# Kernel optimization log

Hardware: AMD Instinct MI355X
Metric: run time of the kernel (lower is better)

Reference implementation:

```python
import jax, jax.numpy as jnp
import numpy as np

NUM_SEQS = 4
SEQ_LEN = 2048
T = NUM_SEQS * SEQ_LEN          # total tokens
D_IN = 4096
D_OUT = 4096
NUM_ADAPTERS = 8
MAX_RANK = 64
CACHE_LEN = NUM_ADAPTERS * MAX_RANK  # 512 pages


def setup_inputs() -> dict:
    key = jax.random.key(0)
    ks = jax.random.split(key, 8)
    x = jax.random.normal(ks[0], (T, D_IN), dtype=jnp.float32)
    weight = jax.random.normal(ks[1], (D_OUT, D_IN), dtype=jnp.float32) * 0.02
    bias = jax.random.normal(ks[2], (D_OUT,), dtype=jnp.float32) * 0.02
    a_cache = jax.random.normal(ks[3], (CACHE_LEN, D_IN), dtype=jnp.float32) * 0.02
    b_cache = jax.random.normal(ks[4], (CACHE_LEN, D_OUT), dtype=jnp.float32) * 0.02
    b_start_loc = (jnp.arange(NUM_SEQS) * SEQ_LEN).astype(jnp.int32)
    b_adapter_ids = jax.random.randint(ks[5], (NUM_SEQS,), 0, NUM_ADAPTERS).astype(jnp.int32)
    b_scaling = jax.random.uniform(ks[6], (NUM_SEQS,), dtype=jnp.float32, minval=0.5, maxval=2.0)
    # page i for (adapter a, rank slot r) lives at a*MAX_RANK + r
    rank_page_table = jnp.arange(CACHE_LEN, dtype=jnp.int32).reshape(NUM_ADAPTERS, MAX_RANK)
    ranks = jax.random.randint(ks[7], (NUM_ADAPTERS,), 1, MAX_RANK + 1).astype(jnp.int32)
    return {"x": x, "weight": weight, "bias": bias, "a_cache": a_cache,
            "b_cache": b_cache, "b_start_loc": b_start_loc,
            "b_adapter_ids": b_adapter_ids, "b_scaling": b_scaling,
            "rank_page_table": rank_page_table, "ranks": ranks}


def reference(x, weight, bias, a_cache, b_cache, b_start_loc,
              b_adapter_ids, b_scaling, rank_page_table, ranks):
    t = x.shape[0]
    num_adapters, max_rank = rank_page_table.shape
    # map each token to its sequence -> adapter id / scaling (mbgmm dispatch)
    seg = jnp.searchsorted(b_start_loc, jnp.arange(t, dtype=b_start_loc.dtype),
                           side='right') - 1                      # [T]
    tok_adapter = b_adapter_ids[seg]                              # [T]
    tok_scale = b_scaling[seg]                                    # [T]
    # gather paged LoRA A/B weights per adapter: [A, R, D]
    A_all = a_cache[rank_page_table]                              # [A, R, D_in]
    B_all = b_cache[rank_page_table]                              # [A, R, D_out]
    # mbgmm_a: xa[t, r] = x[t] . A[adapter(t), r], zero beyond rank
    xa_all = jnp.einsum('td,ard->tar', x, A_all)                  # [T, A, R]
    rmask = (jnp.arange(max_rank)[None, :] < ranks[:, None])      # [A, R]
    onehot = (tok_adapter[:, None] == jnp.arange(num_adapters)[None, :])  # [T, A]
    sel = (onehot[:, :, None] & rmask[None, :, :]).astype(x.dtype)  # [T, A, R]
    xa_sel = xa_all * sel
    # mbgmm_b: lora_out[t] = scaling * sum_r xa[t, r] * B[adapter(t), r]
    lora_out = jnp.einsum('tar,aro->to', xa_sel, B_all) * tok_scale[:, None]
    base_out = x @ weight.T + bias
    return base_out + lora_out
```

## Files before the change

kernel.cpp:

```cpp
#include <hip/hip_runtime.h>
#include <hip/hip_bf16.h>

typedef unsigned short u16;
typedef unsigned int u32;
typedef __attribute__((ext_vector_type(8))) short bf16x8;
typedef __attribute__((ext_vector_type(4))) float f32x4;

#define T_TOK 8192
#define DIN 4096
#define DOUT 4096
#define N_SEQS 4
#define N_ADPT 8
#define MAXR 64
#define CACHE_LEN 512

__device__ __forceinline__ u16 f2bf(float f) {
    u32 u = __builtin_bit_cast(u32, f);
    u += 0x7fffu + ((u >> 16) & 1u);
    return (u16)(u >> 16);
}

__device__ __forceinline__ void load_lds16(const u16* g, u16* l) {
    __builtin_amdgcn_global_load_lds(
        (const __attribute__((address_space(1))) u32*)g,
        (__attribute__((address_space(3))) u32*)l, 16, 0, 0);
}

__global__ void cvt_kernel(const float* __restrict__ in, u16* __restrict__ out, int n4) {
    int i = blockIdx.x * blockDim.x + threadIdx.x;
    int stride = gridDim.x * blockDim.x;
    for (; i < n4; i += stride) {
        float4 v = reinterpret_cast<const float4*>(in)[i];
        ushort4 o;
        o.x = f2bf(v.x); o.y = f2bf(v.y); o.z = f2bf(v.z); o.w = f2bf(v.w);
        reinterpret_cast<ushort4*>(out)[i] = o;
    }
}

__global__ void build_bt(const float* __restrict__ b_cache, const int* __restrict__ rpt,
                         u16* __restrict__ Bt) {
    int id = blockIdx.x * 256 + threadIdx.x;
    int n  = id & (DOUT - 1);
    int rb = (id >> 12) & 7;
    int a  = id >> 15;
    union { u16 u[8]; uint4 v; } pack;
    #pragma unroll
    for (int j = 0; j < 8; ++j) {
        int r = rb * 8 + j;
        int page = rpt[a * MAXR + r];
        pack.u[j] = f2bf(b_cache[(long)page * DOUT + n]);
    }
    *reinterpret_cast<uint4*>(&Bt[((long)(a * DOUT + n)) * MAXR + rb * 8]) = pack.v;
}

__launch_bounds__(256)
__global__ void xa_kernel(const u16* __restrict__ xb, const u16* __restrict__ ab,
                          const int* __restrict__ b_start_loc,
                          const int* __restrict__ b_adapter_ids,
                          const float* __restrict__ b_scaling,
                          const int* __restrict__ rpt,
                          const int* __restrict__ ranks,
                          u16* __restrict__ xa) {
    int t0 = blockIdx.x * 128;
    int seg = 0;
    #pragma unroll
    for (int i = 1; i < N_SEQS; ++i) if (b_start_loc[i] <= t0) seg = i;
    int adapter = b_adapter_ids[seg];
    float scale = b_scaling[seg];
    int rank = ranks[adapter];

    __shared__ __attribute__((aligned(16))) u16 As[128 * 32];
    __shared__ __attribute__((aligned(16))) u16 Bs[64 * 32];

    int tid = threadIdx.x;
    int lane = tid & 63, wave = tid >> 6;
    int lr = lane & 15, lk = lane >> 4;

    int e0 = wave * 64 + lane;
    int e1 = 256 + e0;
    int ra0 = e0 >> 2, ca0 = (e0 & 3) * 8;
    int ra1 = e1 >> 2, ca1 = (e1 & 3) * 8;
    const u16* gA0 = xb + (long)(t0 + ra0) * DIN + ca0;
    const u16* gA1 = xb + (long)(t0 + ra1) * DIN + ca1;
    int rB = ra0;
    int page = rpt[adapter * MAXR + rB];
    const u16* gB = ab + (long)page * DIN + ca0;

    f32x4 acc[2][4] = {};

    for (int k0 = 0; k0 < DIN; k0 += 32) {
        load_lds16(gA0 + k0, As + wave * 512);
        load_lds16(gA1 + k0, As + 2048 + wave * 512);
        load_lds16(gB + k0,  Bs + wave * 512);
        asm volatile("s_waitcnt vmcnt(0)" ::: "memory");
        __syncthreads();
        bf16x8 af[2], bfr[4];
        #pragma unroll
        for (int m = 0; m < 2; ++m)
            af[m] = *(const bf16x8*)&As[(wave * 32 + m * 16 + lr) * 32 + lk * 8];
        #pragma unroll
        for (int n = 0; n < 4; ++n)
            bfr[n] = *(const bf16x8*)&Bs[(n * 16 + lr) * 32 + lk * 8];
        #pragma unroll
        for (int m = 0; m < 2; ++m)
            #pragma unroll
            for (int n = 0; n < 4; ++n)
                acc[m][n] = __builtin_amdgcn_mfma_f32_16x16x32_bf16(af[m], bfr[n], acc[m][n], 0, 0, 0);
        __syncthreads();
    }

    #pragma unroll
    for (int m = 0; m < 2; ++m) {
        int trow = t0 + wave * 32 + m * 16 + lk * 4;
        #pragma unroll
        for (int n = 0; n < 4; ++n) {
            int r = n * 16 + lr;
            #pragma unroll
            for (int j = 0; j < 4; ++j) {
                float v = (r < rank) ? acc[m][n][j] * scale : 0.0f;
                xa[(long)(trow + j) * MAXR + r] = f2bf(v);
            }
        }
    }
}

__launch_bounds__(512, 2)
__global__ void gemm256_kernel(const u16* __restrict__ xb, const u16* __restrict__ wb,
                               const float* __restrict__ bias,
                               const u16* __restrict__ xa, const u16* __restrict__ Bt,
                               const int* __restrict__ b_start_loc,
                               const int* __restrict__ b_adapter_ids,
                               float* __restrict__ out) {
    __shared__ __attribute__((aligned(16))) u16 lds[65536];

    int bid = blockIdx.x;
    int wgid = (bid & 7) * 64 + (bid >> 3);
    int mt = wgid >> 4, nt = wgid & 15;
    int brow = mt * 256, bcol = nt * 256;

    int seg = 0;
    #pragma unroll
    for (int i = 1; i < N_SEQS; ++i) if (b_start_loc[i] <= brow) seg = i;
    int adapter = b_adapter_ids[seg];

    int tid = threadIdx.x;
    int lane = tid & 63, wave = tid >> 6;
    int wm = wave >> 2, wn = wave & 3;
    int lr = lane & 15, lk = lane >> 4;

    int lsw = (tid & 7) ^ ((tid >> 3) & 7);
    int c8  = (lsw & 3) * 8;
    int r0  = (tid >> 3) * 2 + (lsw >> 2);
    const long odA0 = (long)(brow + r0) * DIN + c8;
    const long odA1 = odA0 + 128L * DIN;
    const long odB0 = (long)(bcol + r0) * DIN + c8;
    const long odB1 = odB0 + 128L * DIN;
    const long o6A0 = (long)(brow + r0) * MAXR + c8;
    const long o6A1 = o6A0 + 128L * MAXR;
    const long o6B0 = (long)(adapter * DOUT + bcol + r0) * MAXR + c8;
    const long o6B1 = o6B0 + 128L * MAXR;

    #define STAGE_HALF(T, ks, isB, buf)                                            \
        do {                                                                       \
            u16* d = lds + (buf) * 16384 + (ks) * 8192 + ((isB) ? 32768 : 0) + tid * 8; \
            if ((T) < 64) {                                                        \
                long ko = (long)((T) * 64 + (ks) * 32);                            \
                load_lds16(((isB) ? wb + odB0 : xb + odA0) + ko, d);               \
                load_lds16(((isB) ? wb + odB1 : xb + odA1) + ko, d + 4096);        \
            } else {                                                               \
                long ko = (long)((ks) * 32);                                       \
                load_lds16(((isB) ? Bt + o6B0 : xa + o6A0) + ko, d);               \
                load_lds16(((isB) ? Bt + o6B1 : xa + o6A1) + ko, d + 4096);        \
            }                                                                      \
        } while (0)

    #define LOADA(mh, ks)                                                          \
        _Pragma("unroll")                                                          \
        for (int mi = 0; mi < 4; ++mi) {                                           \
            int r = wm * 128 + (mh) * 64 + mi * 16 + lr;                           \
            int srr = r >> 1;                                                      \
            af[mi] = *(const bf16x8*)&lds[b * 16384 + (ks) * 8192 + srr * 64 +     \
                      ((((r & 1) * 4 + lk) ^ (srr & 7)) * 8)];                     \
        }
    #define LOADB(ks)                                                              \
        _Pragma("unroll")                                                          \
        for (int ni = 0; ni < 4; ++ni) {                                           \
            int r = wn * 64 + ni * 16 + lr;                                        \
            int srr = r >> 1;                                                      \
            bfr[ni] = *(const bf16x8*)&lds[32768 + b * 16384 + (ks) * 8192 + srr * 64 + \
                      ((((r & 1) * 4 + lk) ^ (srr & 7)) * 8)];                     \
        }
    #define MFMA16(mh)                                                             \
        _Pragma("unroll")                                                          \
        for (int mi = 0; mi < 4; ++mi)                                             \
            _Pragma("unroll")                                                      \
            for (int ni = 0; ni < 4; ++ni)                                         \
                acc[(mh) * 4 + mi][ni] = __builtin_amdgcn_mfma_f32_16x16x32_bf16(  \
                    af[mi], bfr[ni], acc[(mh) * 4 + mi][ni], 0, 0, 0);
    #define BAR() do { __builtin_amdgcn_s_barrier(); __builtin_amdgcn_sched_barrier(0); } while (0)

    f32x4 acc[8][4] = {};

    STAGE_HALF(0, 0, false, 0);
    STAGE_HALF(0, 0, true,  0);
    STAGE_HALF(0, 1, false, 0);
    STAGE_HALF(0, 1, true,  0);
    STAGE_HALF(1, 0, true,  1);
    STAGE_HALF(1, 0, false, 1);
    STAGE_HALF(1, 1, true,  1);
    asm volatile("s_waitcnt vmcnt(6)" ::: "memory");
    BAR();

    for (int t = 0; t <= 64; ++t) {
        const int b = t & 1;
        const int t1c = (t + 1 > 64) ? 64 : t + 1;
        const int t2c = (t + 2 > 64) ? 64 : t + 2;
        bf16x8 af[4], bfr[4];

        LOADB(0); LOADA(0, 0);
        STAGE_HALF(t1c, 1, false, (t + 1) & 1);
        BAR();
        __builtin_amdgcn_s_setprio(1); MFMA16(0); __builtin_amdgcn_s_setprio(0);
        BAR();
        LOADA(1, 0);
        STAGE_HALF(t2c, 0, true, b);
        BAR();
        __builtin_amdgcn_s_setprio(1); MFMA16(1); __builtin_amdgcn_s_setprio(0);
        BAR();
        LOADB(1); LOADA(0, 1);
        STAGE_HALF(t2c, 0, false, b);
        BAR();
        __builtin_amdgcn_s_setprio(1); MFMA16(0); __builtin_amdgcn_s_setprio(0);
        BAR();
        LOADA(1, 1);
        STAGE_HALF(t2c, 1, true, b);
        BAR();
        __builtin_amdgcn_s_setprio(1); MFMA16(1); __builtin_amdgcn_s_setprio(0);
        asm volatile("s_waitcnt vmcnt(6)" ::: "memory");
        BAR();
    }
    asm volatile("s_waitcnt vmcnt(0)" ::: "memory");

    #undef STAGE_HALF
    #undef LOADA
    #undef LOADB
    #undef MFMA16
    #undef BAR

    #pragma unroll
    for (int m = 0; m < 8; ++m) {
        int orow = brow + wm * 128 + m * 16 + lk * 4;
        #pragma unroll
        for (int n = 0; n < 4; ++n) {
            int ocol = bcol + wn * 64 + n * 16 + lr;
            float bv = bias[ocol];
            #pragma unroll
            for (int j = 0; j < 4; ++j)
                out[(long)(orow + j) * DOUT + ocol] = acc[m][n][j] + bv;
        }
    }
}

extern "C" void kernel_launch(void* const* d_in, const int* in_sizes, int n_in,
                              void* d_out, int out_size, void* d_ws, size_t ws_size,
                              hipStream_t stream) {
    const float* x          = (const float*)d_in[0];
    const float* weight     = (const float*)d_in[1];
    const float* bias       = (const float*)d_in[2];
    const float* a_cache    = (const float*)d_in[3];
    const float* b_cache    = (const float*)d_in[4];
    const int*   b_start    = (const int*)d_in[5];
    const int*   b_adapter  = (const int*)d_in[6];
    const float* b_scaling  = (const float*)d_in[7];
    const int*   rpt        = (const int*)d_in[8];
    const int*   ranks      = (const int*)d_in[9];
    float* out = (float*)d_out;

    char* ws = (char*)d_ws;
    u16* xb = (u16*)ws; ws += (size_t)T_TOK * DIN * 2;
    u16* wb = (u16*)ws; ws += (size_t)DOUT * DIN * 2;
    u16* ab = (u16*)ws; ws += (size_t)CACHE_LEN * DIN * 2;
    u16* Bt = (u16*)ws; ws += (size_t)N_ADPT * DOUT * MAXR * 2;
    u16* xa = (u16*)ws; ws += (size_t)T_TOK * MAXR * 2;

    cvt_kernel<<<2048, 256, 0, stream>>>(x, xb, T_TOK * DIN / 4);
    cvt_kernel<<<2048, 256, 0, stream>>>(weight, wb, DOUT * DIN / 4);
    cvt_kernel<<<512, 256, 0, stream>>>(a_cache, ab, CACHE_LEN * DIN / 4);
    build_bt<<<(N_ADPT * 8 * DOUT) / 256, 256, 0, stream>>>(b_cache, rpt, Bt);
    xa_kernel<<<T_TOK / 128, 256, 0, stream>>>(xb, ab, b_start, b_adapter, b_scaling, rpt, ranks, xa);
    gemm256_kernel<<<(T_TOK / 256) * (DOUT / 256), 512, 0, stream>>>(xb, wb, bias, xa, Bt, b_start, b_adapter, out);
}
```

Measured before the change: 374.0 us.

## Restructure GEMM main loop to whole-tile prefetch with two barriers per step

```diff
diff --git a/kernel.cpp b/kernel.cpp
--- a/kernel.cpp
+++ b/kernel.cpp
@@ -174,30 +174,14 @@
             }                                                                      \
         } while (0)
 
-    #define LOADA(mh, ks)                                                          \
-        _Pragma("unroll")                                                          \
-        for (int mi = 0; mi < 4; ++mi) {                                           \
-            int r = wm * 128 + (mh) * 64 + mi * 16 + lr;                           \
-            int srr = r >> 1;                                                      \
-            af[mi] = *(const bf16x8*)&lds[b * 16384 + (ks) * 8192 + srr * 64 +     \
-                      ((((r & 1) * 4 + lk) ^ (srr & 7)) * 8)];                     \
-        }
-    #define LOADB(ks)                                                              \
-        _Pragma("unroll")                                                          \
-        for (int ni = 0; ni < 4; ++ni) {                                           \
-            int r = wn * 64 + ni * 16 + lr;                                        \
-            int srr = r >> 1;                                                      \
-            bfr[ni] = *(const bf16x8*)&lds[32768 + b * 16384 + (ks) * 8192 + srr * 64 + \
-                      ((((r & 1) * 4 + lk) ^ (srr & 7)) * 8)];                     \
-        }
-    #define MFMA16(mh)                                                             \
-        _Pragma("unroll")                                                          \
-        for (int mi = 0; mi < 4; ++mi)                                             \
-            _Pragma("unroll")                                                      \
-            for (int ni = 0; ni < 4; ++ni)                                         \
-                acc[(mh) * 4 + mi][ni] = __builtin_amdgcn_mfma_f32_16x16x32_bf16(  \
-                    af[mi], bfr[ni], acc[(mh) * 4 + mi][ni], 0, 0, 0);
-    #define BAR() do { __builtin_amdgcn_s_barrier(); __builtin_amdgcn_sched_barrier(0); } while (0)
+    #define SB0() __builtin_amdgcn_sched_barrier(0)
+    #define BAR() do { __builtin_amdgcn_s_barrier(); SB0(); } while (0)
+    #define DSR(d, p, o) (d) = *(const bf16x8*)((p) + (o))
+
+    const int laneByte = (lr >> 1) * 128 + 16 * ((((lr & 1) << 2) + lk) ^ (lr >> 1));
+    const char* ldsc = (const char*)lds;
+    const int cA = wm * 8192 + laneByte;
+    const int cB = 65536 + wn * 4096 + laneByte;
 
     f32x4 acc[8][4] = {};
 
@@ -205,47 +189,83 @@
     STAGE_HALF(0, 0, true,  0);
     STAGE_HALF(0, 1, false, 0);
     STAGE_HALF(0, 1, true,  0);
-    STAGE_HALF(1, 0, true,  1);
-    STAGE_HALF(1, 0, false, 1);
-    STAGE_HALF(1, 1, true,  1);
-    asm volatile("s_waitcnt vmcnt(6)" ::: "memory");
-    BAR();
 
     for (int t = 0; t <= 64; ++t) {
         const int b = t & 1;
-        const int t1c = (t + 1 > 64) ? 64 : t + 1;
-        const int t2c = (t + 2 > 64) ? 64 : t + 2;
-        bf16x8 af[4], bfr[4];
-
-        LOADB(0); LOADA(0, 0);
-        STAGE_HALF(t1c, 1, false, (t + 1) & 1);
+        if (t < 64) {
+            const int tn = t + 1, bn = tn & 1;
+            STAGE_HALF(tn, 0, false, bn);
+            STAGE_HALF(tn, 0, true,  bn);
+            STAGE_HALF(tn, 1, false, bn);
+            STAGE_HALF(tn, 1, true,  bn);
+            asm volatile("s_waitcnt vmcnt(8)" ::: "memory");
+        } else {
+            asm volatile("s_waitcnt vmcnt(0)" ::: "memory");
+        }
         BAR();
-        __builtin_amdgcn_s_setprio(1); MFMA16(0); __builtin_amdgcn_s_setprio(0);
+
+        const char* pA = ldsc + (b << 15) + cA;
+        const char* pB = ldsc + (b << 15) + cB;
+
+        bf16x8 b0[4], a0[4], a1[4], b1[4], a2[4], a3[4];
+        DSR(b0[0], pB, 0);     DSR(b0[1], pB, 1024);  DSR(b0[2], pB, 2048);  DSR(b0[3], pB, 3072);
+        DSR(a0[0], pA, 0);     DSR(a0[1], pA, 1024);  DSR(a0[2], pA, 2048);  DSR(a0[3], pA, 3072);
+        SB0();
+        DSR(a1[0], pA, 4096);  DSR(a1[1], pA, 5120);  DSR(a1[2], pA, 6144);  DSR(a1[3], pA, 7168);
+        SB0();
+        DSR(b1[0], pB, 16384); DSR(b1[1], pB, 17408); DSR(b1[2], pB, 18432); DSR(b1[3], pB, 19456);
+        DSR(a2[0], pA, 16384); DSR(a2[1], pA, 17408); DSR(a2[2], pA, 18432); DSR(a2[3], pA, 19456);
+        SB0();
+        asm volatile("s_waitcnt lgkmcnt(12)" ::: "memory");
+        SB0();
+        __builtin_amdgcn_s_setprio(1);
+        #pragma unroll
+        for (int mi = 0; mi < 4; ++mi)
+            #pragma unroll
+            for (int ni = 0; ni < 4; ++ni)
+                acc[mi][ni] = __builtin_amdgcn_mfma_f32_16x16x32_bf16(a0[mi], b0[ni], acc[mi][ni], 0, 0, 0);
+        __builtin_amdgcn_s_setprio(0);
+        SB0();
+        DSR(a3[0], pA, 20480); DSR(a3[1], pA, 21504); DSR(a3[2], pA, 22528); DSR(a3[3], pA, 23552);
+        SB0();
+        asm volatile("s_waitcnt lgkmcnt(12)" ::: "memory");
+        SB0();
+        __builtin_amdgcn_s_setprio(1);
+        #pragma unroll
+        for (int mi = 0; mi < 4; ++mi)
+            #pragma unroll
+            for (int ni = 0; ni < 4; ++ni)
+                acc[4 + mi][ni] = __builtin_amdgcn_mfma_f32_16x16x32_bf16(a1[mi], b0[ni], acc[4 + mi][ni], 0, 0, 0);
+        __builtin_amdgcn_s_setprio(0);
+        SB0();
+        asm volatile("s_waitcnt lgkmcnt(4)" ::: "memory");
+        SB0();
+        __builtin_amdgcn_s_setprio(1);
+        #pragma unroll
+        for (int mi = 0; mi < 4; ++mi)
+            #pragma unroll
+            for (int ni = 0; ni < 4; ++ni)
+                acc[mi][ni] = __builtin_amdgcn_mfma_f32_16x16x32_bf16(a2[mi], b1[ni], acc[mi][ni], 0, 0, 0);
+        __builtin_amdgcn_s_setprio(0);
+        SB0();
+        asm volatile("s_waitcnt lgkmcnt(0)" ::: "memory");
+        SB0();
+        __builtin_amdgcn_s_setprio(1);
+        #pragma unroll
+        for (int mi = 0; mi < 4; ++mi)
+            #pragma unroll
+            for (int ni = 0; ni < 4; ++ni)
+                acc[4 + mi][ni] = __builtin_amdgcn_mfma_f32_16x16x32_bf16(a3[mi], b1[ni], acc[4 + mi][ni], 0, 0, 0);
+        __builtin_amdgcn_s_setprio(0);
+        SB0();
+
         BAR();
-        LOADA(1, 0);
-        STAGE_HALF(t2c, 0, true, b);
-        BAR();
-        __builtin_amdgcn_s_setprio(1); MFMA16(1); __builtin_amdgcn_s_setprio(0);
-        BAR();
-        LOADB(1); LOADA(0, 1);
-        STAGE_HALF(t2c, 0, false, b);
-        BAR();
-        __builtin_amdgcn_s_setprio(1); MFMA16(0); __builtin_amdgcn_s_setprio(0);
-        BAR();
-        LOADA(1, 1);
-        STAGE_HALF(t2c, 1, true, b);
-        BAR();
-        __builtin_amdgcn_s_setprio(1); MFMA16(1); __builtin_amdgcn_s_setprio(0);
-        asm volatile("s_waitcnt vmcnt(6)" ::: "memory");
-        BAR();
-    }
-    asm volatile("s_waitcnt vmcnt(0)" ::: "memory");
+    }
 
     #undef STAGE_HALF
-    #undef LOADA
-    #undef LOADB
-    #undef MFMA16
+    #undef SB0
     #undef BAR
+    #undef DSR
 
     #pragma unroll
     for (int m = 0; m < 8; ++m) {
```

Result: slower. 408.0 us (+9.1%).
